# Kernel optimization log

Hardware: AMD Instinct MI355X
Metric: run time of the kernel (lower is better)

Reference implementation:

```python
import jax, jax.numpy as jnp
import numpy as np

B, S, DIM, H = 1, 4096, 1024, 16
HEAD_DIM = DIM // H
ROPE_THETA = 10000.0
LN_EPS = 1e-5


def _rope_cos_sin(seq_len, dim, theta):
    # frequencies over the FULL model dim (rope applied before head split, as in source)
    inv_freq = 1.0 / (theta ** (jnp.arange(0, dim, 2, dtype=jnp.float32) / dim))  # (dim/2,)
    ang = jnp.arange(seq_len, dtype=jnp.float32)[:, None] * inv_freq[None, :]     # (S, dim/2)
    cos = jnp.concatenate([jnp.cos(ang), jnp.cos(ang)], axis=-1)                  # (S, dim)
    sin = jnp.concatenate([jnp.sin(ang), jnp.sin(ang)], axis=-1)
    return cos, sin


def _rotate_half(x):
    d = x.shape[-1] // 2
    return jnp.concatenate([-x[..., d:], x[..., :d]], axis=-1)


def _apply_rope(x, cos, sin):
    # x: (B, S, dim); cos/sin: (S, dim)
    return x * cos[None] + _rotate_half(x) * sin[None]


def setup_inputs() -> dict:
    key = jax.random.key(0)
    ks = jax.random.split(key, 5)
    sc = 1.0 / np.sqrt(DIM)
    return {
        "x": jax.random.normal(ks[0], (B, S, DIM), dtype=jnp.float32),
        "Wqkv": jax.random.normal(ks[1], (DIM, 3 * DIM), dtype=jnp.float32) * sc,
        "bqkv": jax.random.normal(ks[2], (3 * DIM,), dtype=jnp.float32) * 0.01,
        "Wo": jax.random.normal(ks[3], (DIM, DIM), dtype=jnp.float32) * sc,
        "bo": jax.random.normal(ks[4], (DIM,), dtype=jnp.float32) * 0.01,
        "gamma": jnp.ones((DIM,), dtype=jnp.float32),
        "beta": jnp.zeros((DIM,), dtype=jnp.float32),
    }


def reference(x, Wqkv, bqkv, Wo, bo, gamma, beta):
    b, s, d = x.shape
    qkv = x @ Wqkv + bqkv                      # (B, S, 3*dim)
    q, k, v = jnp.split(qkv, 3, axis=-1)       # each (B, S, dim)
    cos, sin = _rope_cos_sin(s, d, ROPE_THETA)
    q = _apply_rope(q, cos, sin)
    k = _apply_rope(k, cos, sin)
    # split heads
    q = q.reshape(b, s, H, HEAD_DIM)
    k = k.reshape(b, s, H, HEAD_DIM)
    v = v.reshape(b, s, H, HEAD_DIM)
    scale = 1.0 / np.sqrt(HEAD_DIM)
    scores = jnp.einsum('bqhd,bkhd->bhqk', q, k) * scale  # (B, H, S, S)
    causal = jnp.triu(jnp.ones((s, s), dtype=bool), k=1)
    scores = jnp.where(causal[None, None], -jnp.inf, scores)
    attn = jax.nn.softmax(scores, axis=-1)
    out = jnp.einsum('bhqk,bkhd->bqhd', attn, v).reshape(b, s, d)
    out = out @ Wo + bo
    # LayerNorm (dropout is identity in eval mode)
    mu = jnp.mean(out, axis=-1, keepdims=True)
    var = jnp.mean(jnp.square(out - mu), axis=-1, keepdims=True)
    return (out - mu) * jax.lax.rsqrt(var + LN_EPS) * gamma + beta
```

## Files before the change

### kernel.cpp

```cpp
#include <hip/hip_runtime.h>
#include <cstdint>
#include <cstddef>

#define S_LEN 4096
#define DIM   1024
#define NH    16
#define HD    64
#define QKV_N 3072
#define NSPLIT 4

typedef __attribute__((ext_vector_type(8))) short short8;
typedef __attribute__((ext_vector_type(4))) float f32x4;
typedef __attribute__((ext_vector_type(16))) float f32x16;
typedef __attribute__((ext_vector_type(4))) unsigned short ushort4v;
typedef __attribute__((ext_vector_type(2))) unsigned int uint2v;
typedef __attribute__((ext_vector_type(4))) unsigned int uint4v;

__device__ inline unsigned short f2bf(float x) {
    unsigned int u = __builtin_bit_cast(unsigned int, x);
    u += 0x7fffu + ((u >> 16) & 1u);
    return (unsigned short)(u >> 16);
}
__device__ inline float bf2f(unsigned short u) {
    return __builtin_bit_cast(float, (unsigned int)u << 16);
}
__device__ inline unsigned int pack2_bf16_rh(float lo, float hi) {
    unsigned int a = __builtin_bit_cast(unsigned int, lo) + 0x8000u;
    unsigned int b = __builtin_bit_cast(unsigned int, hi) + 0x8000u;
    return __builtin_amdgcn_perm(b, a, 0x07060302u);
}

__device__ inline void gl_lds16(const void* g, void* l) {
    __builtin_amdgcn_global_load_lds(
        (const __attribute__((address_space(1))) void*)g,
        (__attribute__((address_space(3))) void*)l, 16, 0, 0);
}

__global__ __launch_bounds__(256) void gemm_mfma_kernel(
    const unsigned short* __restrict__ A,
    const unsigned short* __restrict__ Bt,
    const float* __restrict__ bias,
    unsigned short* __restrict__ C,
    int M, int N, int K)
{
    __shared__ unsigned short As[128 * 32];
    __shared__ unsigned short Bs[128 * 32];

    const int t    = threadIdx.x;
    const int w    = t >> 6;
    const int lane = t & 63;
    const int ln   = lane & 15;
    const int quad = lane >> 4;
    const int bm   = blockIdx.y * 128;
    const int bn   = blockIdx.x * 128;
    const int wm   = (w & 1) * 64;
    const int wn   = (w >> 1) * 64;

    f32x4 acc[4][4];
#pragma unroll
    for (int i = 0; i < 4; ++i)
#pragma unroll
        for (int j = 0; j < 4; ++j) acc[i][j] = (f32x4){0.f, 0.f, 0.f, 0.f};

    const int lr = lane >> 2;
    const int lc = (lane & 3) * 8;
    const unsigned short* ga = A  + (size_t)(bm + w * 32 + lr) * K + lc;
    const unsigned short* gb = Bt + (size_t)(bn + w * 32 + lr) * K + lc;
    unsigned short* la = &As[(w * 32) * 32];
    unsigned short* lb = &Bs[(w * 32) * 32];

    for (int k0 = 0; k0 < K; k0 += 32) {
        gl_lds16(ga,            la);
        gl_lds16(ga + 16 * K,   la + 16 * 32);
        gl_lds16(gb,            lb);
        gl_lds16(gb + 16 * K,   lb + 16 * 32);
        ga += 32; gb += 32;
        __syncthreads();

        short8 af[4], bf[4];
#pragma unroll
        for (int i = 0; i < 4; ++i)
            af[i] = *(const short8*)&As[(wm + i * 16 + ln) * 32 + quad * 8];
#pragma unroll
        for (int j = 0; j < 4; ++j)
            bf[j] = *(const short8*)&Bs[(wn + j * 16 + ln) * 32 + quad * 8];
#pragma unroll
        for (int i = 0; i < 4; ++i)
#pragma unroll
            for (int j = 0; j < 4; ++j)
                acc[i][j] = __builtin_amdgcn_mfma_f32_16x16x32_bf16(af[i], bf[j], acc[i][j], 0, 0, 0);
        __syncthreads();
    }

#pragma unroll
    for (int j = 0; j < 4; ++j) {
        const int col = bn + wn + j * 16 + ln;
        const float bv = bias[col];
#pragma unroll
        for (int i = 0; i < 4; ++i) {
            const int row0 = bm + wm + i * 16 + quad * 4;
#pragma unroll
            for (int r = 0; r < 4; ++r)
                C[(size_t)(row0 + r) * N + col] = f2bf(acc[i][j][r] + bv);
        }
    }
}

__global__ __launch_bounds__(256) void gemm_mfma_splitk_kernel(
    const unsigned short* __restrict__ A,
    const unsigned short* __restrict__ Bt,
    float* __restrict__ P,
    int M, int N, int K)
{
    __shared__ unsigned short As[128 * 32];
    __shared__ unsigned short Bs[128 * 32];

    const int t    = threadIdx.x;
    const int w    = t >> 6;
    const int lane = t & 63;
    const int ln   = lane & 15;
    const int quad = lane >> 4;
    const int bm   = blockIdx.y * 128;
    const int bn   = blockIdx.x * 128;
    const int z    = blockIdx.z;
    const int wm   = (w & 1) * 64;
    const int wn   = (w >> 1) * 64;
    const int kh   = K >> 1;

    f32x4 acc[4][4];
#pragma unroll
    for (int i = 0; i < 4; ++i)
#pragma unroll
        for (int j = 0; j < 4; ++j) acc[i][j] = (f32x4){0.f, 0.f, 0.f, 0.f};

    const int lr = lane >> 2;
    const int lc = (lane & 3) * 8;
    const unsigned short* ga = A  + (size_t)(bm + w * 32 + lr) * K + z * kh + lc;
    const unsigned short* gb = Bt + (size_t)(bn + w * 32 + lr) * K + z * kh + lc;
    unsigned short* la = &As[(w * 32) * 32];
    unsigned short* lb = &Bs[(w * 32) * 32];

    for (int k0 = 0; k0 < kh; k0 += 32) {
        gl_lds16(ga,            la);
        gl_lds16(ga + 16 * K,   la + 16 * 32);
        gl_lds16(gb,            lb);
        gl_lds16(gb + 16 * K,   lb + 16 * 32);
        ga += 32; gb += 32;
        __syncthreads();

        short8 af[4], bf[4];
#pragma unroll
        for (int i = 0; i < 4; ++i)
            af[i] = *(const short8*)&As[(wm + i * 16 + ln) * 32 + quad * 8];
#pragma unroll
        for (int j = 0; j < 4; ++j)
            bf[j] = *(const short8*)&Bs[(wn + j * 16 + ln) * 32 + quad * 8];
#pragma unroll
        for (int i = 0; i < 4; ++i)
#pragma unroll
            for (int j = 0; j < 4; ++j)
                acc[i][j] = __builtin_amdgcn_mfma_f32_16x16x32_bf16(af[i], bf[j], acc[i][j], 0, 0, 0);
        __syncthreads();
    }

    float* Pz = P + (size_t)z * M * N;
#pragma unroll
    for (int j = 0; j < 4; ++j) {
        const int col = bn + wn + j * 16 + ln;
#pragma unroll
        for (int i = 0; i < 4; ++i) {
            const int row0 = bm + wm + i * 16 + quad * 4;
#pragma unroll
            for (int r = 0; r < 4; ++r)
                Pz[(size_t)(row0 + r) * N + col] = acc[i][j][r];
        }
    }
}

__global__ __launch_bounds__(256) void prep1_kernel(
    const float* __restrict__ x, unsigned short* __restrict__ xb,
    const float* __restrict__ Wqkv, unsigned short* __restrict__ WqkvT,
    const float* __restrict__ Wo, unsigned short* __restrict__ WoT)
{
    __shared__ unsigned short L[64][72];
    const int b = blockIdx.x;
    const int t = threadIdx.x;

    if (b < 2048) {
        const size_t i = ((size_t)b * 256 + t) * 8;
        float4 a = *(const float4*)(x + i);
        float4 c = *(const float4*)(x + i + 4);
        short8 p = { (short)f2bf(a.x), (short)f2bf(a.y), (short)f2bf(a.z), (short)f2bf(a.w),
                     (short)f2bf(c.x), (short)f2bf(c.y), (short)f2bf(c.z), (short)f2bf(c.w) };
        *(short8*)(xb + i) = p;
        return;
    }
    const float* W;
    unsigned short* Wt;
    int N, n0, k0;
    if (b < 2816) {
        const int wb = b - 2048;
        W = Wqkv; Wt = WqkvT; N = QKV_N;
        n0 = (wb % 48) * 64; k0 = (wb / 48) * 64;
    } else {
        const int wb = b - 2816;
        W = Wo; Wt = WoT; N = DIM;
        n0 = (wb & 15) * 64; k0 = (wb >> 4) * 64;
    }
    const int kr = t >> 2, cb = (t & 3) * 16;
    const float* wp = W + (size_t)(k0 + kr) * N + n0 + cb;
#pragma unroll
    for (int u = 0; u < 16; u += 4) {
        float4 v = *(const float4*)(wp + u);
        ushort4v p = { f2bf(v.x), f2bf(v.y), f2bf(v.z), f2bf(v.w) };
        *(ushort4v*)&L[kr][cb + u] = p;
    }
    __syncthreads();
    const int nr = t >> 2, kb = (t & 3) * 16;
    short8 lo, hi;
#pragma unroll
    for (int u = 0; u < 8; ++u) lo[u] = (short)L[kb + u][nr];
#pragma unroll
    for (int u = 0; u < 8; ++u) hi[u] = (short)L[kb + 8 + u][nr];
    unsigned short* op = Wt + (size_t)(n0 + nr) * 1024 + k0 + kb;
    *(short8*)op       = lo;
    *(short8*)(op + 8) = hi;
}

__global__ __launch_bounds__(256) void prep2_kernel(
    const unsigned short* __restrict__ qkvb,
    unsigned short* __restrict__ Qb,
    unsigned short* __restrict__ Kb,
    unsigned short* __restrict__ Vt)
{
    __shared__ unsigned short L[64][72];
    const int b = blockIdx.x;
    const int t = threadIdx.x;

    if (b < 2048) {
        const int idx = b * 256 + t;
        const int j   = (idx & 127) * 4;
        const int s   = idx >> 7;
        const unsigned short* row = qkvb + (size_t)s * QKV_N;
        unsigned short* qo = Qb + (size_t)s * DIM;
        unsigned short* ko = Kb + (size_t)s * DIM;
        const float sf = (float)s;
        const float QSCALE = 0.18033688011112042f;
        const float C1 = -0.025952563241307517f;
        const float INV2PI = 0.15915494309189535f;

        float cs[4], sn[4];
#pragma unroll
        for (int e = 0; e < 4; ++e) {
            const float invf2pi = exp2f((float)(j + e) * C1) * INV2PI;
            float rev = sf * invf2pi;
            rev -= floorf(rev);
            sn[e] = __builtin_amdgcn_sinf(rev);
            cs[e] = __builtin_amdgcn_cosf(rev);
        }
        ushort4v q1 = *(const ushort4v*)(row + j);
        ushort4v q2 = *(const ushort4v*)(row + 512 + j);
        ushort4v k1 = *(const ushort4v*)(row + DIM + j);
        ushort4v k2 = *(const ushort4v*)(row + DIM + 512 + j);
        ushort4v qa, qb4, ka, kb4;
#pragma unroll
        for (int e = 0; e < 4; ++e) {
            const float x1 = bf2f(q1[e]), x2 = bf2f(q2[e]);
            const float y1 = bf2f(k1[e]), y2 = bf2f(k2[e]);
            qa[e]  = f2bf((x1 * cs[e] - x2 * sn[e]) * QSCALE);
            qb4[e] = f2bf((x2 * cs[e] + x1 * sn[e]) * QSCALE);
            ka[e]  = f2bf(y1 * cs[e] - y2 * sn[e]);
            kb4[e] = f2bf(y2 * cs[e] + y1 * sn[e]);
        }
        *(ushort4v*)(qo + j)       = qa;
        *(ushort4v*)(qo + 512 + j) = qb4;
        *(ushort4v*)(ko + j)       = ka;
        *(ushort4v*)(ko + 512 + j) = kb4;
        return;
    }

    const int vb = b - 2048;
    const int c0 = (vb & 15) * 64;
    const int bs = (vb >> 4) * 64;
    const int sl = t >> 2, cb = (t & 3) * 16;
    const unsigned short* vp = qkvb + (size_t)(bs + sl) * QKV_N + 2 * DIM + c0 + cb;
    *(short8*)&L[sl][cb]     = *(const short8*)vp;
    *(short8*)&L[sl][cb + 8] = *(const short8*)(vp + 8);
    __syncthreads();
    const int cl = t >> 2, sb = (t & 3) * 16;
    short8 lo, hi;
#pragma unroll
    for (int u = 0; u < 8; ++u) lo[u] = (short)L[sb + u][cl];
#pragma unroll
    for (int u = 0; u < 8; ++u) hi[u] = (short)L[sb + 8 + u][cl];
    unsigned short* op = Vt + (size_t)(c0 + cl) * S_LEN + bs + sb;
    *(short8*)op       = lo;
    *(short8*)(op + 8) = hi;
}

__global__ __launch_bounds__(256) void attn_mfma_kernel(
    const unsigned short* __restrict__ Qb,
    const unsigned short* __restrict__ Kb,
    const unsigned short* __restrict__ Vt,
    unsigned short* __restrict__ Opb,
    float* __restrict__ lp)
{
    __shared__ unsigned short Ks[2][64 * 64];
    __shared__ unsigned short Vs[2][64 * 64];

    const int t    = threadIdx.x;
    const int w    = t >> 6;
    const int lane = t & 63;
    const int r31  = lane & 31;
    const int hi   = lane >> 5;
    const int p    = blockIdx.x;
    const int spl  = blockIdx.y;
    const int h    = blockIdx.z;

    const int srow  = t >> 2;
    const int sch   = (t & 3) * 2;
    const int ssw   = srow & 7;
    const int soff0 = srow * 64 + ((sch ^ ssw) << 3);
    const int soff1 = srow * 64 + (((sch + 1) ^ ssw) << 3);

    const int rA = r31 * 64;
    const int sw = r31 & 7;

#pragma unroll
    for (int phase = 0; phase < 2; ++phase) {
        const int qt  = phase == 0 ? (31 - p) : p;
        const int q0  = qt * 128;
        const int nkt = 2 * qt + 2;
        const int kt_begin = (nkt * spl) / NSPLIT;
        const int kt_end   = (nkt * (spl + 1)) / NSPLIT;

        short8 qf[4];
        {
            const unsigned short* qp = Qb + (size_t)(q0 + w * 32 + r31) * DIM + h * HD + hi * 8;
#pragma unroll
            for (int kk = 0; kk < 4; ++kk) qf[kk] = *(const short8*)(qp + kk * 16);
        }

        f32x16 o0 = {}, o1 = {};
        float lrow = 0.f;

        short8 kr0, kr1, vr0, vr1;
        {
            const int k0 = kt_begin * 64;
            const unsigned short* kp = Kb + (size_t)(k0 + srow) * DIM + h * HD + sch * 8;
            kr0 = *(const short8*)kp;  kr1 = *(const short8*)(kp + 8);
            const unsigned short* vp = Vt + (size_t)(h * HD + srow) * S_LEN + k0 + sch * 8;
            vr0 = *(const short8*)vp;  vr1 = *(const short8*)(vp + 8);
        }
        __syncthreads();

        for (int kt = kt_begin; kt < kt_end; ++kt) {
            const int buf = (kt - kt_begin) & 1;
            unsigned short* ks = &Ks[buf][0];
            unsigned short* vs = &Vs[buf][0];
            *(short8*)&ks[soff0] = kr0;
            *(short8*)&ks[soff1] = kr1;
            *(short8*)&vs[soff0] = vr0;
            *(short8*)&vs[soff1] = vr1;
            if (kt + 1 < kt_end) {
                const int k1 = (kt + 1) * 64;
                const unsigned short* kp = Kb + (size_t)(k1 + srow) * DIM + h * HD + sch * 8;
                kr0 = *(const short8*)kp;  kr1 = *(const short8*)(kp + 8);
                const unsigned short* vp = Vt + (size_t)(h * HD + srow) * S_LEN + k1 + sch * 8;
                vr0 = *(const short8*)vp;  vr1 = *(const short8*)(vp + 8);
            }
            __syncthreads();

            f32x16 s0 = {}, s1 = {};
            __builtin_amdgcn_s_setprio(1);
#pragma unroll
            for (int kk = 0; kk < 4; ++kk) {
                const int co = (((kk * 2 + hi) ^ sw) << 3);
                short8 kf0 = *(const short8*)&ks[rA + co];
                short8 kf1 = *(const short8*)&ks[rA + 2048 + co];
                s0 = __builtin_amdgcn_mfma_f32_32x32x16_bf16(kf0, qf[kk], s0, 0, 0, 0);
                s1 = __builtin_amdgcn_mfma_f32_32x32x16_bf16(kf1, qf[kk], s1, 0, 0, 0);
            }
            __builtin_amdgcn_s_setprio(0);

            if (kt >= nkt - 2) {
                const int qg = q0 + w * 32 + r31;
                const int kb = kt * 64 + 4 * hi;
#pragma unroll
                for (int g = 0; g < 4; ++g)
#pragma unroll
                    for (int a = 0; a < 4; ++a) {
                        const int keyl = kb + a + 8 * g;
                        if (keyl > qg)      s0[4 * g + a] = -1e30f;
                        if (keyl + 32 > qg) s1[4 * g + a] = -1e30f;
                    }
            }

            unsigned int pd0[8], pd1[8];
            float ps = 0.f;
#pragma unroll
            for (int g = 0; g < 4; ++g) {
                const float a0 = __builtin_amdgcn_exp2f(s0[4 * g + 0]);
                const float a1 = __builtin_amdgcn_exp2f(s0[4 * g + 1]);
                const float a2 = __builtin_amdgcn_exp2f(s0[4 * g + 2]);
                const float a3 = __builtin_amdgcn_exp2f(s0[4 * g + 3]);
                const float b0 = __builtin_amdgcn_exp2f(s1[4 * g + 0]);
                const float b1 = __builtin_amdgcn_exp2f(s1[4 * g + 1]);
                const float b2 = __builtin_amdgcn_exp2f(s1[4 * g + 2]);
                const float b3 = __builtin_amdgcn_exp2f(s1[4 * g + 3]);
                ps += ((a0 + a1) + (a2 + a3)) + ((b0 + b1) + (b2 + b3));
                pd0[2 * g]     = pack2_bf16_rh(a0, a1);
                pd0[2 * g + 1] = pack2_bf16_rh(a2, a3);
                pd1[2 * g]     = pack2_bf16_rh(b0, b1);
                pd1[2 * g + 1] = pack2_bf16_rh(b2, b3);
            }
            ps += __shfl_xor(ps, 32);
            lrow += ps;

#pragma unroll
            for (int w16 = 0; w16 < 4; ++w16) {
                const int lw = w16 & 1;
                unsigned int a0, b0, a1, b1;
                if (w16 < 2) { a0 = pd0[4 * lw];     b0 = pd0[4 * lw + 2];
                               a1 = pd0[4 * lw + 1]; b1 = pd0[4 * lw + 3]; }
                else         { a0 = pd1[4 * lw];     b0 = pd1[4 * lw + 2];
                               a1 = pd1[4 * lw + 1]; b1 = pd1[4 * lw + 3]; }
                asm("v_permlane32_swap_b32 %0, %1" : "+v"(a0), "+v"(b0));
                asm("v_permlane32_swap_b32 %0, %1" : "+v"(a1), "+v"(b1));
                const uint4v frw = { a0, a1, b0, b1 };
                const short8 pf = __builtin_bit_cast(short8, frw);
                const int co = (((w16 * 2 + hi) ^ sw) << 3);
                short8 vf0 = *(const short8*)&vs[rA + co];
                short8 vf1 = *(const short8*)&vs[rA + 2048 + co];
                __builtin_amdgcn_s_setprio(1);
                o0 = __builtin_amdgcn_mfma_f32_32x32x16_bf16(vf0, pf, o0, 0, 0, 0);
                o1 = __builtin_amdgcn_mfma_f32_32x32x16_bf16(vf1, pf, o1, 0, 0, 0);
                __builtin_amdgcn_s_setprio(0);
            }
        }

        {
            unsigned short* op = Opb + ((size_t)spl * S_LEN + q0 + w * 32 + r31) * DIM + h * HD + hi * 4;
#pragma unroll
            for (int g = 0; g < 4; ++g) {
                ushort4v v0 = { f2bf(o0[4 * g + 0]), f2bf(o0[4 * g + 1]),
                                f2bf(o0[4 * g + 2]), f2bf(o0[4 * g + 3]) };
                ushort4v v1 = { f2bf(o1[4 * g + 0]), f2bf(o1[4 * g + 1]),
                                f2bf(o1[4 * g + 2]), f2bf(o1[4 * g + 3]) };
                *(ushort4v*)(op + g * 8)      = v0;
                *(ushort4v*)(op + 32 + g * 8) = v1;
            }
            if (hi == 0)
                lp[((size_t)spl * NH + h) * S_LEN + q0 + w * 32 + r31] = lrow;
        }
    }
}

__global__ __launch_bounds__(256) void combine_kernel(
    const unsigned short* __restrict__ Opb, const float* __restrict__ lp,
    unsigned short* __restrict__ attnb)
{
    const int row = blockIdx.x;
    const int t   = threadIdx.x;
    const int d   = t * 4;
    const int h   = t >> 4;
    float acc[4] = {0.f, 0.f, 0.f, 0.f};
    float l = 0.f;
#pragma unroll
    for (int s = 0; s < NSPLIT; ++s) {
        ushort4v a = *(const ushort4v*)&Opb[((size_t)s * S_LEN + row) * DIM + d];
#pragma unroll
        for (int e = 0; e < 4; ++e) acc[e] += bf2f(a[e]);
        l += lp[((size_t)s * NH + h) * S_LEN + row];
    }
    const float inv = 1.0f / l;
    ushort4v o;
#pragma unroll
    for (int e = 0; e < 4; ++e) o[e] = f2bf(acc[e] * inv);
    *(ushort4v*)&attnb[(size_t)row * DIM + d] = o;
}

__global__ __launch_bounds__(256) void ln_kernel(
    const float* __restrict__ p0, const float* __restrict__ p1,
    const float* __restrict__ bo, const float* __restrict__ gamma,
    const float* __restrict__ beta, float* __restrict__ out)
{
    const int row = blockIdx.x;
    const int t = threadIdx.x;
    const float4 a = *(const float4*)&p0[(size_t)row * DIM + t * 4];
    const float4 c = *(const float4*)&p1[(size_t)row * DIM + t * 4];
    const float4 bb = *(const float4*)&bo[t * 4];
    const float4 v = { a.x + c.x + bb.x, a.y + c.y + bb.y,
                       a.z + c.z + bb.z, a.w + c.w + bb.w };
    float s  = v.x + v.y + v.z + v.w;
    float sq = v.x * v.x + v.y * v.y + v.z * v.z + v.w * v.w;
#pragma unroll
    for (int off = 1; off < 64; off <<= 1) {
        s  += __shfl_xor(s, off);
        sq += __shfl_xor(sq, off);
    }
    __shared__ float red[8];
    const int wv = t >> 6, ln = t & 63;
    if (ln == 0) { red[wv] = s; red[4 + wv] = sq; }
    __syncthreads();
    s  = red[0] + red[1] + red[2] + red[3];
    sq = red[4] + red[5] + red[6] + red[7];
    const float mu  = s * (1.0f / DIM);
    const float var = sq * (1.0f / DIM) - mu * mu;
    const float rs  = rsqrtf(var + 1e-5f);
    const float4 g = *(const float4*)&gamma[t * 4];
    const float4 b = *(const float4*)&beta[t * 4];
    float4 o = { (v.x - mu) * rs * g.x + b.x,
                 (v.y - mu) * rs * g.y + b.y,
                 (v.z - mu) * rs * g.z + b.z,
                 (v.w - mu) * rs * g.w + b.w };
    *(float4*)&out[(size_t)row * DIM + t * 4] = o;
}

extern "C" void kernel_launch(void* const* d_in, const int* in_sizes, int n_in,
                              void* d_out, int out_size, void* d_ws, size_t ws_size,
                              hipStream_t stream)
{
    const float* x     = (const float*)d_in[0];
    const float* Wqkv  = (const float*)d_in[1];
    const float* bqkv  = (const float*)d_in[2];
    const float* Wo    = (const float*)d_in[3];
    const float* bo    = (const float*)d_in[4];
    const float* gamma = (const float*)d_in[5];
    const float* beta  = (const float*)d_in[6];
    float* out = (float*)d_out;

    char* base = (char*)d_ws;
    unsigned short* qkvb  = (unsigned short*)base;
    unsigned short* attnb = (unsigned short*)base;
    unsigned short* Opb   = (unsigned short*)(base + (size_t)8 * 1024 * 1024);
    float* proj = (float*)(base + (size_t)8 * 1024 * 1024);
    float* lp   = (float*)(base + (size_t)40 * 1024 * 1024);
    unsigned short* Qb    = (unsigned short*)(base + (size_t)48 * 1024 * 1024);
    unsigned short* Kb    = (unsigned short*)(base + (size_t)56 * 1024 * 1024);
    unsigned short* Vt    = (unsigned short*)(base + (size_t)64 * 1024 * 1024);
    unsigned short* xb    = (unsigned short*)(base + (size_t)72 * 1024 * 1024);
    unsigned short* WqkvT = (unsigned short*)(base + (size_t)80 * 1024 * 1024);
    unsigned short* WoT   = (unsigned short*)(base + (size_t)86 * 1024 * 1024);

    prep1_kernel<<<3072, 256, 0, stream>>>(x, xb, Wqkv, WqkvT, Wo, WoT);

    gemm_mfma_kernel<<<dim3(QKV_N / 128, S_LEN / 128), 256, 0, stream>>>(
        xb, WqkvT, bqkv, qkvb, S_LEN, QKV_N, DIM);

    prep2_kernel<<<3072, 256, 0, stream>>>(qkvb, Qb, Kb, Vt);

    attn_mfma_kernel<<<dim3(16, NSPLIT, NH), 256, 0, stream>>>(Qb, Kb, Vt, Opb, lp);

    combine_kernel<<<S_LEN, 256, 0, stream>>>(Opb, lp, attnb);

    gemm_mfma_splitk_kernel<<<dim3(DIM / 128, S_LEN / 128, 2), 256, 0, stream>>>(
        attnb, WoT, proj, S_LEN, DIM, DIM);

    ln_kernel<<<S_LEN, 256, 0, stream>>>(proj, proj + (size_t)S_LEN * DIM, bo,
                                         gamma, beta, out);
}
```

Measured before the change: 242.0 us.

## Fuse V transpose into QKV GEMM, XCD-aware tiling, bf16 split-K partials

The QKV GEMM now writes V directly in transposed layout from its epilogue, so the V-transpose path in prep2 goes away. Both GEMMs use a 1D grid remapped so each XCD gets a contiguous band of M tiles, for better L2 locality. The output-projection split-K partials are stored as bf16 instead of fp32, halving that traffic at some precision cost. Attention split count drops from 4 to 2, and the s_setprio hints around the MFMAs are removed.

```diff
diff --git a/kernel.cpp b/kernel.cpp
--- a/kernel.cpp
+++ b/kernel.cpp
@@ -7,13 +7,12 @@
 #define NH    16
 #define HD    64
 #define QKV_N 3072
-#define NSPLIT 4
+#define NSPLIT 2
 
 typedef __attribute__((ext_vector_type(8))) short short8;
 typedef __attribute__((ext_vector_type(4))) float f32x4;
 typedef __attribute__((ext_vector_type(16))) float f32x16;
 typedef __attribute__((ext_vector_type(4))) unsigned short ushort4v;
-typedef __attribute__((ext_vector_type(2))) unsigned int uint2v;
 typedef __attribute__((ext_vector_type(4))) unsigned int uint4v;
 
 __device__ inline unsigned short f2bf(float x) {
@@ -41,18 +40,23 @@
     const unsigned short* __restrict__ Bt,
     const float* __restrict__ bias,
     unsigned short* __restrict__ C,
+    unsigned short* __restrict__ Vt,
     int M, int N, int K)
 {
     __shared__ unsigned short As[128 * 32];
     __shared__ unsigned short Bs[128 * 32];
 
+    const int nbn  = N >> 7;
+    const int mper = (M >> 7) >> 3;
+    const int c    = blockIdx.x >> 3;
+    const int xcd  = blockIdx.x & 7;
+    const int bm   = (xcd * mper + (c % mper)) * 128;
+    const int bn   = (c / mper) * 128;
     const int t    = threadIdx.x;
     const int w    = t >> 6;
     const int lane = t & 63;
     const int ln   = lane & 15;
     const int quad = lane >> 4;
-    const int bm   = blockIdx.y * 128;
-    const int bn   = blockIdx.x * 128;
     const int wm   = (w & 1) * 64;
     const int wn   = (w >> 1) * 64;
 
@@ -92,6 +96,22 @@
         __syncthreads();
     }
 
+    if (bn >= 2 * DIM) {
+#pragma unroll
+        for (int j = 0; j < 4; ++j) {
+            const int col  = bn + wn + j * 16 + ln;
+            const int colp = col - 2 * DIM;
+            const float bv = bias[col];
+#pragma unroll
+            for (int i = 0; i < 4; ++i) {
+                const int row0 = bm + wm + i * 16 + quad * 4;
+                ushort4v v = { f2bf(acc[i][j][0] + bv), f2bf(acc[i][j][1] + bv),
+                               f2bf(acc[i][j][2] + bv), f2bf(acc[i][j][3] + bv) };
+                *(ushort4v*)&Vt[(size_t)colp * S_LEN + row0] = v;
+            }
+        }
+        return;
+    }
 #pragma unroll
     for (int j = 0; j < 4; ++j) {
         const int col = bn + wn + j * 16 + ln;
@@ -106,23 +126,29 @@
     }
 }
 
-__global__ __launch_bounds__(256) void gemm_mfma_splitk_kernel(
+__global__ __launch_bounds__(256) void gemm_proj_splitk_kernel(
     const unsigned short* __restrict__ A,
     const unsigned short* __restrict__ Bt,
-    float* __restrict__ P,
+    unsigned short* __restrict__ P,
     int M, int N, int K)
 {
     __shared__ unsigned short As[128 * 32];
     __shared__ unsigned short Bs[128 * 32];
 
+    const int nbn  = N >> 7;
+    const int mper = (M >> 7) >> 3;
+    const int cpx  = mper * nbn * 2;
+    const int c    = blockIdx.x >> 3;
+    const int xcd  = blockIdx.x & 7;
+    const int bm   = (xcd * mper + (c % mper)) * 128;
+    const int rem  = c / mper;
+    const int bn   = (rem & 7) * 128;
+    const int z    = rem >> 3;
     const int t    = threadIdx.x;
     const int w    = t >> 6;
     const int lane = t & 63;
     const int ln   = lane & 15;
     const int quad = lane >> 4;
-    const int bm   = blockIdx.y * 128;
-    const int bn   = blockIdx.x * 128;
-    const int z    = blockIdx.z;
     const int wm   = (w & 1) * 64;
     const int wn   = (w >> 1) * 64;
     const int kh   = K >> 1;
@@ -163,7 +189,7 @@
         __syncthreads();
     }
 
-    float* Pz = P + (size_t)z * M * N;
+    unsigned short* Pz = P + (size_t)z * M * N;
 #pragma unroll
     for (int j = 0; j < 4; ++j) {
         const int col = bn + wn + j * 16 + ln;
@@ -172,7 +198,7 @@
             const int row0 = bm + wm + i * 16 + quad * 4;
 #pragma unroll
             for (int r = 0; r < 4; ++r)
-                Pz[(size_t)(row0 + r) * N + col] = acc[i][j][r];
+                Pz[(size_t)(row0 + r) * N + col] = f2bf(acc[i][j][r]);
         }
     }
 }
@@ -230,72 +256,49 @@
 __global__ __launch_bounds__(256) void prep2_kernel(
     const unsigned short* __restrict__ qkvb,
     unsigned short* __restrict__ Qb,
-    unsigned short* __restrict__ Kb,
-    unsigned short* __restrict__ Vt)
-{
-    __shared__ unsigned short L[64][72];
+    unsigned short* __restrict__ Kb)
+{
     const int b = blockIdx.x;
     const int t = threadIdx.x;
 
-    if (b < 2048) {
-        const int idx = b * 256 + t;
-        const int j   = (idx & 127) * 4;
-        const int s   = idx >> 7;
-        const unsigned short* row = qkvb + (size_t)s * QKV_N;
-        unsigned short* qo = Qb + (size_t)s * DIM;
-        unsigned short* ko = Kb + (size_t)s * DIM;
-        const float sf = (float)s;
-        const float QSCALE = 0.18033688011112042f;
-        const float C1 = -0.025952563241307517f;
-        const float INV2PI = 0.15915494309189535f;
-
-        float cs[4], sn[4];
-#pragma unroll
-        for (int e = 0; e < 4; ++e) {
-            const float invf2pi = exp2f((float)(j + e) * C1) * INV2PI;
-            float rev = sf * invf2pi;
-            rev -= floorf(rev);
-            sn[e] = __builtin_amdgcn_sinf(rev);
-            cs[e] = __builtin_amdgcn_cosf(rev);
-        }
-        ushort4v q1 = *(const ushort4v*)(row + j);
-        ushort4v q2 = *(const ushort4v*)(row + 512 + j);
-        ushort4v k1 = *(const ushort4v*)(row + DIM + j);
-        ushort4v k2 = *(const ushort4v*)(row + DIM + 512 + j);
-        ushort4v qa, qb4, ka, kb4;
-#pragma unroll
-        for (int e = 0; e < 4; ++e) {
-            const float x1 = bf2f(q1[e]), x2 = bf2f(q2[e]);
-            const float y1 = bf2f(k1[e]), y2 = bf2f(k2[e]);
-            qa[e]  = f2bf((x1 * cs[e] - x2 * sn[e]) * QSCALE);
-            qb4[e] = f2bf((x2 * cs[e] + x1 * sn[e]) * QSCALE);
-            ka[e]  = f2bf(y1 * cs[e] - y2 * sn[e]);
-            kb4[e] = f2bf(y2 * cs[e] + y1 * sn[e]);
-        }
-        *(ushort4v*)(qo + j)       = qa;
-        *(ushort4v*)(qo + 512 + j) = qb4;
-        *(ushort4v*)(ko + j)       = ka;
-        *(ushort4v*)(ko + 512 + j) = kb4;
-        return;
-    }
-
-    const int vb = b - 2048;
-    const int c0 = (vb & 15) * 64;
-    const int bs = (vb >> 4) * 64;
-    const int sl = t >> 2, cb = (t & 3) * 16;
-    const unsigned short* vp = qkvb + (size_t)(bs + sl) * QKV_N + 2 * DIM + c0 + cb;
-    *(short8*)&L[sl][cb]     = *(const short8*)vp;
-    *(short8*)&L[sl][cb + 8] = *(const short8*)(vp + 8);
-    __syncthreads();
-    const int cl = t >> 2, sb = (t & 3) * 16;
-    short8 lo, hi;
-#pragma unroll
-    for (int u = 0; u < 8; ++u) lo[u] = (short)L[sb + u][cl];
-#pragma unroll
-    for (int u = 0; u < 8; ++u) hi[u] = (short)L[sb + 8 + u][cl];
-    unsigned short* op = Vt + (size_t)(c0 + cl) * S_LEN + bs + sb;
-    *(short8*)op       = lo;
-    *(short8*)(op + 8) = hi;
+    const int idx = b * 256 + t;
+    const int j   = (idx & 127) * 4;
+    const int s   = idx >> 7;
+    const unsigned short* row = qkvb + (size_t)s * QKV_N;
+    unsigned short* qo = Qb + (size_t)s * DIM;
+    unsigned short* ko = Kb + (size_t)s * DIM;
+    const float sf = (float)s;
+    const float QSCALE = 0.18033688011112042f;
+    const float C1 = -0.025952563241307517f;
+    const float INV2PI = 0.15915494309189535f;
+
+    float cs[4], sn[4];
+#pragma unroll
+    for (int e = 0; e < 4; ++e) {
+        const float invf2pi = exp2f((float)(j + e) * C1) * INV2PI;
+        float rev = sf * invf2pi;
+        rev -= floorf(rev);
+        sn[e] = __builtin_amdgcn_sinf(rev);
+        cs[e] = __builtin_amdgcn_cosf(rev);
+    }
+    ushort4v q1 = *(const ushort4v*)(row + j);
+    ushort4v q2 = *(const ushort4v*)(row + 512 + j);
+    ushort4v k1 = *(const ushort4v*)(row + DIM + j);
+    ushort4v k2 = *(const ushort4v*)(row + DIM + 512 + j);
+    ushort4v qa, qb4, ka, kb4;
+#pragma unroll
+    for (int e = 0; e < 4; ++e) {
+        const float x1 = bf2f(q1[e]), x2 = bf2f(q2[e]);
+        const float y1 = bf2f(k1[e]), y2 = bf2f(k2[e]);
+        qa[e]  = f2bf((x1 * cs[e] - x2 * sn[e]) * QSCALE);
+        qb4[e] = f2bf((x2 * cs[e] + x1 * sn[e]) * QSCALE);
+        ka[e]  = f2bf(y1 * cs[e] - y2 * sn[e]);
+        kb4[e] = f2bf(y2 * cs[e] + y1 * sn[e]);
+    }
+    *(ushort4v*)(qo + j)       = qa;
+    *(ushort4v*)(qo + 512 + j) = qb4;
+    *(ushort4v*)(ko + j)       = ka;
+    *(ushort4v*)(ko + 512 + j) = kb4;
 }
 
 __global__ __launch_bounds__(256) void attn_mfma_kernel(
@@ -372,7 +375,6 @@
             __syncthreads();
 
             f32x16 s0 = {}, s1 = {};
-            __builtin_amdgcn_s_setprio(1);
 #pragma unroll
             for (int kk = 0; kk < 4; ++kk) {
                 const int co = (((kk * 2 + hi) ^ sw) << 3);
@@ -381,7 +383,6 @@
                 s0 = __builtin_amdgcn_mfma_f32_32x32x16_bf16(kf0, qf[kk], s0, 0, 0, 0);
                 s1 = __builtin_amdgcn_mfma_f32_32x32x16_bf16(kf1, qf[kk], s1, 0, 0, 0);
             }
-            __builtin_amdgcn_s_setprio(0);
 
             if (kt >= nkt - 2) {
                 const int qg = q0 + w * 32 + r31;
@@ -432,10 +433,8 @@
                 const int co = (((w16 * 2 + hi) ^ sw) << 3);
                 short8 vf0 = *(const short8*)&vs[rA + co];
                 short8 vf1 = *(const short8*)&vs[rA + 2048 + co];
-                __builtin_amdgcn_s_setprio(1);
                 o0 = __builtin_amdgcn_mfma_f32_32x32x16_bf16(vf0, pf, o0, 0, 0, 0);
                 o1 = __builtin_amdgcn_mfma_f32_32x32x16_bf16(vf1, pf, o1, 0, 0, 0);
-                __builtin_amdgcn_s_setprio(0);
             }
         }
 
@@ -481,17 +480,19 @@
 }
 
 __global__ __launch_bounds__(256) void ln_kernel(
-    const float* __restrict__ p0, const float* __restrict__ p1,
+    const unsigned short* __restrict__ p0, const unsigned short* __restrict__ p1,
     const float* __restrict__ bo, const float* __restrict__ gamma,
     const float* __restrict__ beta, float* __restrict__ out)
 {
     const int row = blockIdx.x;
     const int t = threadIdx.x;
-    const float4 a = *(const float4*)&p0[(size_t)row * DIM + t * 4];
-    const float4 c = *(const float4*)&p1[(size_t)row * DIM + t * 4];
+    const ushort4v a = *(const ushort4v*)&p0[(size_t)row * DIM + t * 4];
+    const ushort4v c = *(const ushort4v*)&p1[(size_t)row * DIM + t * 4];
     const float4 bb = *(const float4*)&bo[t * 4];
-    const float4 v = { a.x + c.x + bb.x, a.y + c.y + bb.y,
-                       a.z + c.z + bb.z, a.w + c.w + bb.w };
+    const float4 v = { bf2f(a[0]) + bf2f(c[0]) + bb.x,
+                       bf2f(a[1]) + bf2f(c[1]) + bb.y,
+                       bf2f(a[2]) + bf2f(c[2]) + bb.z,
+                       bf2f(a[3]) + bf2f(c[3]) + bb.w };
     float s  = v.x + v.y + v.z + v.w;
     float sq = v.x * v.x + v.y * v.y + v.z * v.z + v.w * v.w;
 #pragma unroll
@@ -534,7 +535,7 @@
     unsigned short* qkvb  = (unsigned short*)base;
     unsigned short* attnb = (unsigned short*)base;
     unsigned short* Opb   = (unsigned short*)(base + (size_t)8 * 1024 * 1024);
-    float* proj = (float*)(base + (size_t)8 * 1024 * 1024);
+    unsigned short* projP = (unsigned short*)(base + (size_t)8 * 1024 * 1024);
     float* lp   = (float*)(base + (size_t)40 * 1024 * 1024);
     unsigned short* Qb    = (unsigned short*)(base + (size_t)48 * 1024 * 1024);
     unsigned short* Kb    = (unsigned short*)(base + (size_t)56 * 1024 * 1024);
@@ -545,18 +546,18 @@
 
     prep1_kernel<<<3072, 256, 0, stream>>>(x, xb, Wqkv, WqkvT, Wo, WoT);
 
-    gemm_mfma_kernel<<<dim3(QKV_N / 128, S_LEN / 128), 256, 0, stream>>>(
-        xb, WqkvT, bqkv, qkvb, S_LEN, QKV_N, DIM);
-
-    prep2_kernel<<<3072, 256, 0, stream>>>(qkvb, Qb, Kb, Vt);
+    gemm_mfma_kernel<<<768, 256, 0, stream>>>(
+        xb, WqkvT, bqkv, qkvb, Vt, S_LEN, QKV_N, DIM);
+
+    prep2_kernel<<<2048, 256, 0, stream>>>(qkvb, Qb, Kb);
 
     attn_mfma_kernel<<<dim3(16, NSPLIT, NH), 256, 0, stream>>>(Qb, Kb, Vt, Opb, lp);
 
     combine_kernel<<<S_LEN, 256, 0, stream>>>(Opb, lp, attnb);
 
-    gemm_mfma_splitk_kernel<<<dim3(DIM / 128, S_LEN / 128, 2), 256, 0, stream>>>(
-        attnb, WoT, proj, S_LEN, DIM, DIM);
-
-    ln_kernel<<<S_LEN, 256, 0, stream>>>(proj, proj + (size_t)S_LEN * DIM, bo,
+    gemm_proj_splitk_kernel<<<512, 256, 0, stream>>>(
+        attnb, WoT, projP, S_LEN, DIM, DIM);
+
+    ln_kernel<<<S_LEN, 256, 0, stream>>>(projP, projP + (size_t)S_LEN * DIM, bo,
                                          gamma, beta, out);
 }
```

After: 235.1 us. 1.03x faster.
